# Optimization experiments

Hardware: AMD Instinct MI355X
Metric: run time of the kernel (lower is better)

## Reference

```python
import jax, jax.numpy as jnp
import numpy as np

B, N, D, C, H, W = 4, 900, 256, 256, 200, 200
HEADS, LVLS, PTS, K = 8, 1, 4, 10


def setup_inputs() -> dict:
    key = jax.random.key(0)
    ks = jax.random.split(key, 16)
    s = 0.02
    return {
        "query_embed": jax.random.normal(ks[0], (B, N, D), jnp.float32),
        "ctrl_points": jax.random.uniform(ks[1], (B, N, 4, 2), jnp.float32, -50.0, 50.0),
        "bev_features": jax.random.normal(ks[2], (B, C, H, W), jnp.float32),
        "spatial_shapes": jnp.array([[H, W]], dtype=jnp.int32),
        "pc_range": jnp.array([-51.2, -51.2, -5.0, 51.2, 51.2, 3.0], jnp.float32),
        "Wq": s * jax.random.normal(ks[3], (D, D)), "bq": jnp.zeros((D,)),
        "Wv": s * jax.random.normal(ks[4], (C, D)), "bv": jnp.zeros((D,)),
        "Woff": s * jax.random.normal(ks[5], (D, HEADS * LVLS * PTS * 2)), "boff": jnp.zeros((HEADS * LVLS * PTS * 2,)),
        "Wattn": s * jax.random.normal(ks[6], (D, HEADS * LVLS * PTS)), "battn": jnp.zeros((HEADS * LVLS * PTS,)),
        "Wmo": s * jax.random.normal(ks[7], (D, D)), "bmo": jnp.zeros((D,)),
        "Wo": s * jax.random.normal(ks[8], (D, D)), "bo": jnp.zeros((D,)),
    }


def _forward(query_embed, ctrl_points, bev_features, spatial_shapes, pc_range,
             Wq, bq, Wv, bv, Woff, boff, Wattn, battn, Wmo, bmo, Wo, bo):
    b, n, d = query_embed.shape
    _, c, h, w = bev_features.shape
    hd = d // HEADS

    # --- cubic Bezier interpolation: (B,N,4,2) -> (B,N,K,2) dense points ---
    t = jnp.linspace(0.0, 1.0, K, dtype=query_embed.dtype)
    basis = jnp.stack([(1 - t) ** 3, 3 * (1 - t) ** 2 * t, 3 * (1 - t) * t ** 2, t ** 3], axis=-1)  # (K,4)
    dense = jnp.einsum('kc,bncd->bnkd', basis, ctrl_points)
    # --- normalize to [0,1] by pc_range, clamp to [0.01,0.99] ---
    nx = (dense[..., 0] - pc_range[0]) / (pc_range[3] - pc_range[0])
    ny = (dense[..., 1] - pc_range[1]) / (pc_range[4] - pc_range[1])
    ref = jnp.clip(jnp.stack([nx, ny], axis=-1), 0.01, 0.99)  # (B,N,K,2)

    # --- projections ---
    q = query_embed @ Wq + bq                                       # (B,N,D) (identity for residual)
    v = bev_features.reshape(b, c, h * w).transpose(0, 2, 1) @ Wv + bv  # (B,HW,D)
    v = v.reshape(b, h * w, HEADS, hd)

    off = (q @ Woff + boff).reshape(b, n, HEADS, LVLS, PTS, 2)
    aw = jax.nn.softmax((q @ Wattn + battn).reshape(b, n, HEADS, LVLS * PTS), axis=-1)
    aw = aw.reshape(b, n, HEADS, PTS)  # LVLS == 1

    # offset normalizer = (W, H) per level
    normalizer = jnp.stack([spatial_shapes[..., 1], spatial_shapes[..., 0]], axis=-1).astype(q.dtype)  # (L,2)
    # sampling locations: broadcast K bezier points against heads/points offsets
    loc = ref[:, :, None, :, None, :] + off / normalizer[None, None, None, :, None, :]  # (B,N,HEADS,K,PTS,2)

    # --- bilinear sampling, align_corners=False, zero padding ---
    gx = loc[..., 0] * w - 0.5
    gy = loc[..., 1] * h - 0.5
    x0 = jnp.floor(gx)
    y0 = jnp.floor(gy)
    wx = gx - x0
    wy = gy - y0
    x0i = x0.astype(jnp.int32)
    y0i = y0.astype(jnp.int32)

    vflat = v.transpose(0, 2, 1, 3).reshape(b * HEADS, h * w, hd)  # (B*HEADS, HW, hd)

    def flat(a):  # (B,N,HEADS,K,PTS) -> (B*HEADS, N*K*PTS)
        return a.transpose(0, 2, 1, 3, 4).reshape(b * HEADS, n * K * PTS)

    acc = jnp.zeros((b * HEADS, n * K * PTS, hd), dtype=q.dtype)
    for dx, dy in ((0, 0), (1, 0), (0, 1), (1, 1)):
        ix = flat(x0i) + dx
        iy = flat(y0i) + dy
        wxx = flat(wx) if dx else (1.0 - flat(wx))
        wyy = flat(wy) if dy else (1.0 - flat(wy))
        valid = (ix >= 0) & (ix < w) & (iy >= 0) & (iy < h)
        idx = jnp.clip(iy, 0, h - 1) * w + jnp.clip(ix, 0, w - 1)
        corner = jnp.take_along_axis(vflat, idx[..., None], axis=1)  # (B*HEADS, Npts, hd)
        acc = acc + corner * (wxx * wyy * valid.astype(q.dtype))[..., None]

    sampled = acc.reshape(b, HEADS, n, K, PTS, hd)
    # weighted sum over (K, PTS); attention weights shared across the K bezier points
    out = jnp.einsum('bhnkpd,bnhp->bnhd', sampled, aw).reshape(b, n, d)
    out = out @ Wmo + bmo + q   # mmcv MSDeformAttn output_proj + residual (identity = query)
    out = out @ Wo + bo         # outer output_proj
    return out


def reference(query_embed, ctrl_points, bev_features, spatial_shapes, pc_range,
              Wq, bq, Wv, bv, Woff, boff, Wattn, battn, Wmo, bmo, Wo, bo):
    return _forward(query_embed, ctrl_points, bev_features, spatial_shapes, pc_range,
                    Wq, bq, Wv, bv, Woff, boff, Wattn, battn, Wmo, bmo, Wo, bo)
```

## Files before the change

kernel.cpp:

```cpp
#include <hip/hip_runtime.h>
#include <hip/hip_bf16.h>
#include <math.h>


typedef unsigned short u16;
typedef unsigned int u32;
typedef short bf16x8 __attribute__((ext_vector_type(8)));
typedef float f32x4 __attribute__((ext_vector_type(4)));

__device__ __forceinline__ float bflo(u32 w) {
  union { u32 i; float f; } c; c.i = w << 16; return c.f;
}
__device__ __forceinline__ float bfhi(u32 w) {
  union { u32 i; float f; } c; c.i = w & 0xffff0000u; return c.f;
}
__device__ __forceinline__ u16 f2bf(float f) {
  union { float f; u32 i; } c; c.f = f;
  u32 u = c.i;
  return (u16)((u + 0x7FFFu + ((u >> 16) & 1u)) >> 16);
}
__device__ __forceinline__ int imin(int a, int b) { return a < b ? a : b; }
__device__ __forceinline__ int imax(int a, int b) { return a > b ? a : b; }

__device__ __forceinline__ void glds16(const u16* g, u16* l) {
  __builtin_amdgcn_global_load_lds(
      (__attribute__((address_space(1))) const void*)g,
      (__attribute__((address_space(3))) void*)l, 16, 0, 0);
}

__global__ __launch_bounds__(256) void prep_weights(
    const float* __restrict__ Wq, const float* __restrict__ Wv,
    const float* __restrict__ Woff, const float* __restrict__ Wattn,
    const float* __restrict__ Wmo, const float* __restrict__ Wo,
    const float* __restrict__ bq, const float* __restrict__ boff,
    const float* __restrict__ battn, const float* __restrict__ bmo,
    const float* __restrict__ bo, const float* __restrict__ query,
    u16* __restrict__ bqoaT, u16* __restrict__ wvT, u16* __restrict__ woCat,
    float* __restrict__ bcat, float* __restrict__ bprime,
    u16* __restrict__ qin)
{
  const int idx = blockIdx.x * 256 + threadIdx.x;
  {
    int i = idx * 4;
    float4 v = *(const float4*)(query + i);
    uint2 st;
    st.x = (u32)f2bf(v.x) | ((u32)f2bf(v.y) << 16);
    st.y = (u32)f2bf(v.z) | ((u32)f2bf(v.w) << 16);
    *(uint2*)(qin + i) = st;
  }
  if (idx < 65536) {
    int r = idx >> 8, c = idx & 255;
    bqoaT[idx] = f2bf(Wq[c * 256 + r]);
    wvT[idx]   = f2bf(Wv[c * 256 + r]);
  }
  if (idx < 24576) {
    int n = idx >> 8, k = idx & 255;
    const float* wq = Wq + k * 256;
    float s = 0.f;
    if (n < 64) {
      const float* wo = Woff + n;
#pragma unroll 4
      for (int c = 0; c < 256; c += 4) {
        float4 a = *(const float4*)(wq + c);
        s += a.x * wo[(c + 0) * 64] + a.y * wo[(c + 1) * 64] +
             a.z * wo[(c + 2) * 64] + a.w * wo[(c + 3) * 64];
      }
    } else {
      const float* wa = Wattn + (n - 64);
#pragma unroll 4
      for (int c = 0; c < 256; c += 4) {
        float4 a = *(const float4*)(wq + c);
        s += a.x * wa[(c + 0) * 32] + a.y * wa[(c + 1) * 32] +
             a.z * wa[(c + 2) * 32] + a.w * wa[(c + 3) * 32];
      }
    }
    bqoaT[65536 + idx] = f2bf(s);
  }
  if (idx < 131072) {
    int n = idx >> 9, k = idx & 511;
    float s;
    if (k >= 256) {
      s = Wo[(size_t)(k - 256) * 256 + n];
    } else {
      const float* wm = Wmo + k * 256;
      const float* wo = Wo + n;
      s = 0.f;
#pragma unroll 4
      for (int c = 0; c < 256; c += 4) {
        float4 a = *(const float4*)(wm + c);
        s += a.x * wo[(c + 0) * 256] + a.y * wo[(c + 1) * 256] +
             a.z * wo[(c + 2) * 256] + a.w * wo[(c + 3) * 256];
      }
    }
    woCat[idx] = f2bf(s);
  }
  if (idx >= 131072 && idx < 131328) {
    int n = idx - 131072;
    const float* wo = Wo + n;
    float s = bo[n];
    for (int c = 0; c < 256; ++c) s += bmo[c] * wo[c * 256];
    bprime[n] = s;
  }
  if (idx >= 131328 && idx < 131680) {
    int n = idx - 131328;
    if (n < 256) {
      bcat[n] = bq[n];
    } else {
      int j = n - 256;
      float s;
      if (j < 64) {
        const float* wo = Woff + j;
        s = boff[j];
        for (int c = 0; c < 256; ++c) s += bq[c] * wo[c * 64];
      } else {
        const float* wa = Wattn + (j - 64);
        s = battn[j - 64];
        for (int c = 0; c < 256; ++c) s += bq[c] * wa[c * 32];
      }
      bcat[n] = s;
    }
  }
}

enum { GM_F32 = 0, GM_SPLIT = 1 };

template <int MODE>
__global__ __launch_bounds__(256) void gemm_bt(
    const u16* __restrict__ A, const u16* __restrict__ Bt,
    const float* __restrict__ bias,
    u16* __restrict__ outb, float* __restrict__ outf,
    int M, int N, int K, int lda, int ldo)
{
  __shared__ __align__(16) u16 lA[128 * 32];
  __shared__ __align__(16) u16 lB[128 * 32];
  const int tid = threadIdx.x;
  const int wv = tid >> 6, lane = tid & 63;
  const int m0 = blockIdx.y * 128;
  const int n0 = blockIdx.x * 128;

  const int crow = lane >> 2;
  const int ckoff = (lane & 3) * 8;
  const int a1 = imin(m0 + wv * 16 + crow, M - 1);
  const int a2 = imin(m0 + (wv + 4) * 16 + crow, M - 1);
  const int b1 = imin(n0 + wv * 16 + crow, N - 1);
  const int b2 = imin(n0 + (wv + 4) * 16 + crow, N - 1);
  const u16* gA1 = A + (size_t)a1 * lda + ckoff;
  const u16* gA2 = A + (size_t)a2 * lda + ckoff;
  const u16* gB1 = Bt + (size_t)b1 * K + ckoff;
  const u16* gB2 = Bt + (size_t)b2 * K + ckoff;
  u16* lA1 = lA + wv * 512;  u16* lA2 = lA + (wv + 4) * 512;
  u16* lB1 = lB + wv * 512;  u16* lB2 = lB + (wv + 4) * 512;

  const int fm = (wv & 1) * 64, fn = (wv >> 1) * 64;
  const int fr = lane & 15, fk = (lane >> 4) * 8;

  f32x4 acc[4][4];
#pragma unroll
  for (int i = 0; i < 4; ++i)
#pragma unroll
    for (int j = 0; j < 4; ++j) acc[i][j] = (f32x4){0.f, 0.f, 0.f, 0.f};

  for (int k0 = 0; k0 < K; k0 += 32) {
    glds16(gA1 + k0, lA1);
    glds16(gA2 + k0, lA2);
    glds16(gB1 + k0, lB1);
    glds16(gB2 + k0, lB2);
    __syncthreads();
    bf16x8 af[4], bfv[4];
#pragma unroll
    for (int i = 0; i < 4; ++i)
      af[i] = *(const bf16x8*)&lA[(fm + i * 16 + fr) * 32 + fk];
#pragma unroll
    for (int j = 0; j < 4; ++j)
      bfv[j] = *(const bf16x8*)&lB[(fn + j * 16 + fr) * 32 + fk];
    __syncthreads();
#pragma unroll
    for (int i = 0; i < 4; ++i)
#pragma unroll
      for (int j = 0; j < 4; ++j)
        acc[i][j] = __builtin_amdgcn_mfma_f32_16x16x32_bf16(af[i], bfv[j], acc[i][j], 0, 0, 0);
  }

  const int quad = lane >> 4;
#pragma unroll
  for (int j = 0; j < 4; ++j) {
    const int n = n0 + fn + j * 16 + fr;
    const bool nok = (n < N);
    const float bcol = bias[nok ? n : 0];
#pragma unroll
    for (int i = 0; i < 4; ++i) {
      const int mb = m0 + fm + i * 16 + quad * 4;
#pragma unroll
      for (int r = 0; r < 4; ++r) {
        const int m = mb + r;
        if (m < M && nok) {
          float x = acc[i][j][r] + bcol;
          if (MODE == GM_F32) {
            outf[(size_t)m * ldo + n] = x;
          } else {
            if (n < 256) outb[(size_t)m * 512 + n] = f2bf(x);
            else outf[(size_t)m * 96 + (n - 256)] = x;
          }
        }
      }
    }
  }
}

#define LOADB(S, R0, R1, R2, R3)                                   \
  { const float* s2_ = src + (size_t)((S) * 32) * 40000;           \
    R0 = *(const float4*)(s2_);                                    \
    R1 = *(const float4*)(s2_ + 4);                                \
    R2 = *(const float4*)(s2_ + 40000);                            \
    R3 = *(const float4*)(s2_ + 40004); }

#define CVW8F(BUF, R0, R1, R2, R3)                                           \
  { u32* lbw_ = (u32*)(BUF); u32 pk_;                                        \
    asm("v_cvt_pk_bf16_f32 %0, %1, %2" : "=v"(pk_) : "v"(R0.x), "v"(R2.x)); \
    lbw_[(((wrow + 0) * 16 + wslot) ^ wxor)] = pk_;                          \
    asm("v_cvt_pk_bf16_f32 %0, %1, %2" : "=v"(pk_) : "v"(R0.y), "v"(R2.y)); \
    lbw_[(((wrow + 1) * 16 + wslot) ^ wxor)] = pk_;                          \
    asm("v_cvt_pk_bf16_f32 %0, %1, %2" : "=v"(pk_) : "v"(R0.z), "v"(R2.z)); \
    lbw_[(((wrow + 2) * 16 + wslot) ^ wxor)] = pk_;                          \
    asm("v_cvt_pk_bf16_f32 %0, %1, %2" : "=v"(pk_) : "v"(R0.w), "v"(R2.w)); \
    lbw_[(((wrow + 3) * 16 + wslot) ^ wxor)] = pk_;                          \
    asm("v_cvt_pk_bf16_f32 %0, %1, %2" : "=v"(pk_) : "v"(R1.x), "v"(R3.x)); \
    lbw_[(((wrow + 4) * 16 + wslot) ^ wxor)] = pk_;                          \
    asm("v_cvt_pk_bf16_f32 %0, %1, %2" : "=v"(pk_) : "v"(R1.y), "v"(R3.y)); \
    lbw_[(((wrow + 5) * 16 + wslot) ^ wxor)] = pk_;                          \
    asm("v_cvt_pk_bf16_f32 %0, %1, %2" : "=v"(pk_) : "v"(R1.z), "v"(R3.z)); \
    lbw_[(((wrow + 6) * 16 + wslot) ^ wxor)] = pk_;                          \
    asm("v_cvt_pk_bf16_f32 %0, %1, %2" : "=v"(pk_) : "v"(R1.w), "v"(R3.w)); \
    lbw_[(((wrow + 7) * 16 + wslot) ^ wxor)] = pk_; }

__global__ __launch_bounds__(256) void gemm_v4(
    const u16* __restrict__ A,
    const float* __restrict__ bev,
    const float* __restrict__ bias,
    u16* __restrict__ outb,
    int zbase)
{
  const int tid = threadIdx.x;
  const int wv = tid >> 6, lane = tid & 63;
  const int z = zbase + blockIdx.y;
  const int w = blockIdx.x * 4 + wv;
  if (w >= 1250) return;
  const int nw0 = w * 32;
  const int fr = lane & 15, fk = (lane >> 4) * 8;

  const float* bsrc = bev + ((size_t)z * 256 + fk) * 40000 + nw0 + fr;
  const u16* asrc = A + (size_t)fr * 256 + fk;

  f32x4 acc[16][2];
#pragma unroll
  for (int i = 0; i < 16; ++i) {
    acc[i][0] = (f32x4){0.f, 0.f, 0.f, 0.f};
    acc[i][1] = (f32x4){0.f, 0.f, 0.f, 0.f};
  }

#pragma unroll
  for (int t = 0; t < 8; ++t) {
    const float* bs = bsrc + (size_t)(t * 32) * 40000;
    float b0[8], b1[8];
#pragma unroll
    for (int j = 0; j < 8; ++j) {
      b0[j] = bs[(size_t)j * 40000];
      b1[j] = bs[(size_t)j * 40000 + 16];
    }
    union { u32 u[4]; bf16x8 v; } p0, p1;
#pragma unroll
    for (int j = 0; j < 4; ++j) {
      asm("v_cvt_pk_bf16_f32 %0, %1, %2"
          : "=v"(p0.u[j]) : "v"(b0[2 * j]), "v"(b0[2 * j + 1]));
      asm("v_cvt_pk_bf16_f32 %0, %1, %2"
          : "=v"(p1.u[j]) : "v"(b1[2 * j]), "v"(b1[2 * j + 1]));
    }
#pragma unroll
    for (int i = 0; i < 16; ++i) {
      bf16x8 af = *(const bf16x8*)(asrc + i * 4096 + t * 32);
      acc[i][0] = __builtin_amdgcn_mfma_f32_16x16x32_bf16(af, p0.v, acc[i][0], 0, 0, 0);
      acc[i][1] = __builtin_amdgcn_mfma_f32_16x16x32_bf16(af, p1.v, acc[i][1], 0, 0, 0);
    }
  }

  const int quad = lane >> 4;
#pragma unroll
  for (int i = 0; i < 16; ++i) {
    const int mb = i * 16 + quad * 4;
#pragma unroll
    for (int j = 0; j < 2; ++j) {
      const int n = nw0 + j * 16 + fr;
      u16 u0 = f2bf(acc[i][j][0] + bias[mb + 0]);
      u16 u1 = f2bf(acc[i][j][1] + bias[mb + 1]);
      u16 u2 = f2bf(acc[i][j][2] + bias[mb + 2]);
      u16 u3 = f2bf(acc[i][j][3] + bias[mb + 3]);
      size_t off = (size_t)z * (8ull * 40000 * 32) +
                   (size_t)(mb >> 5) * (40000 * 32) + (size_t)n * 32 + (mb & 31);
      uint2 st; st.x = (u32)u0 | ((u32)u1 << 16); st.y = (u32)u2 | ((u32)u3 << 16);
      *(uint2*)(outb + off) = st;
    }
  }
}

__global__ __launch_bounds__(256, 2) void gemm_v(
    const u16* __restrict__ A, const float* __restrict__ bev,
    const float* __restrict__ bias, u16* __restrict__ outb, int zbase)
{
  __shared__ __align__(16) u16 lA[8 * 128 * 32];
  __shared__ __align__(16) u16 lB[2][128 * 32];
  const int tid = threadIdx.x;
  const int wv = tid >> 6, lane = tid & 63;
  const int m0 = blockIdx.x * 128;
  const int n0 = blockIdx.y * 128;
  const int z = zbase + blockIdx.z;

  const int crow = lane >> 2, ckoff = (lane & 3) * 8;
  const u16* gA1 = A + (size_t)(m0 + wv * 16 + crow) * 256 + ckoff;
  const u16* gA2 = A + (size_t)(m0 + (wv + 4) * 16 + crow) * 256 + ckoff;
  u16* lA1 = lA + wv * 512;
  u16* lA2 = lA + (wv + 4) * 512;

  const int kp = tid >> 4, nb = tid & 15;
  const int cb = imin(n0 + nb * 8, 40000 - 8);
  const float* src = bev + ((size_t)z * 256 + 2 * kp) * 40000 + cb;
  const int wslot = (((kp >> 2) ^ (nb & 3)) << 2) + (kp & 3);
  const int wxor = ((nb >> 2) & 1) << 4;
  const int wrow = nb * 8;

  const int fm = (wv & 1) * 64, fn = (wv >> 1) * 64;
  const int fr = lane & 15, fk = (lane >> 4) * 8;

  f32x4 acc[4][4];
#pragma unroll
  for (int i = 0; i < 4; ++i)
#pragma unroll
    for (int j = 0; j < 4; ++j) acc[i][j] = (f32x4){0.f, 0.f, 0.f, 0.f};

  float4 s0a, s0b, s0c, s0d, s1a, s1b, s1c, s1d;
  float4 s2a, s2b, s2c, s2d, s3a, s3b, s3c, s3d;

  LOADB(0, s0a, s0b, s0c, s0d);
#pragma unroll
  for (int s = 0; s < 8; ++s) {
    glds16(gA1 + s * 32, lA1 + s * 4096);
    glds16(gA2 + s * 32, lA2 + s * 4096);
  }
  LOADB(1, s1a, s1b, s1c, s1d);
  LOADB(2, s2a, s2b, s2c, s2d);
  LOADB(3, s3a, s3b, s3c, s3d);
  asm volatile("" ::: "memory");
  CVW8F(lB[0], s0a, s0b, s0c, s0d);
  __syncthreads();

#pragma unroll
  for (int t = 0; t < 8; ++t) {
    bf16x8 af[4], bfv[4];
#pragma unroll
    for (int i = 0; i < 4; ++i)
      af[i] = *(const bf16x8*)&lA[t * 4096 + (fm + i * 16 + fr) * 32 + fk];
#pragma unroll
    for (int j = 0; j < 4; ++j) {
      const int n = fn + j * 16 + fr;
      const int pc = (((lane >> 4) ^ ((n >> 3) & 3)) << 3);
      const int ri = (n * 32 + pc) ^ (((n >> 5) & 1) << 5);
      bfv[j] = *(const bf16x8*)&lB[t & 1][ri];
    }
    if (t == 0)      { LOADB(4, s0a, s0b, s0c, s0d); }
    else if (t == 1) { LOADB(5, s1a, s1b, s1c, s1d); }
    else if (t == 2) { LOADB(6, s2a, s2b, s2c, s2d); }
    else if (t == 3) { LOADB(7, s3a, s3b, s3c, s3d); }
    if (t == 0)      { CVW8F(lB[1], s1a, s1b, s1c, s1d); }
    else if (t == 1) { CVW8F(lB[0], s2a, s2b, s2c, s2d); }
    else if (t == 2) { CVW8F(lB[1], s3a, s3b, s3c, s3d); }
    else if (t == 3) { CVW8F(lB[0], s0a, s0b, s0c, s0d); }
    else if (t == 4) { CVW8F(lB[1], s1a, s1b, s1c, s1d); }
    else if (t == 5) { CVW8F(lB[0], s2a, s2b, s2c, s2d); }
    else if (t == 6) { CVW8F(lB[1], s3a, s3b, s3c, s3d); }
#pragma unroll
    for (int i = 0; i < 4; ++i)
#pragma unroll
      for (int j = 0; j < 4; ++j)
        acc[i][j] = __builtin_amdgcn_mfma_f32_16x16x32_bf16(af[i], bfv[j], acc[i][j], 0, 0, 0);
    if (t < 7) {
      __builtin_amdgcn_sched_barrier(0);
      asm volatile("s_waitcnt lgkmcnt(0)" ::: "memory");
      __builtin_amdgcn_sched_barrier(0);
      __builtin_amdgcn_s_barrier();
      __builtin_amdgcn_sched_barrier(0);
    }
  }

  const int quad = lane >> 4;
#pragma unroll
  for (int j = 0; j < 4; ++j) {
    const int n = n0 + fn + j * 16 + fr;
    if (n < 40000) {
#pragma unroll
      for (int i = 0; i < 4; ++i) {
        const int mb = m0 + fm + i * 16 + quad * 4;
        u16 u0 = f2bf(acc[i][j][0] + bias[mb + 0]);
        u16 u1 = f2bf(acc[i][j][1] + bias[mb + 1]);
        u16 u2 = f2bf(acc[i][j][2] + bias[mb + 2]);
        u16 u3 = f2bf(acc[i][j][3] + bias[mb + 3]);
        size_t off = (size_t)z * (8ull * 40000 * 32) +
                     (size_t)(mb >> 5) * (40000 * 32) + (size_t)n * 32 + (mb & 31);
        uint2 st; st.x = (u32)u0 | ((u32)u1 << 16); st.y = (u32)u2 | ((u32)u3 << 16);
        *(uint2*)(outb + off) = st;
      }
    }
  }
}

__global__ __launch_bounds__(256) void sampler(
    const float* __restrict__ ctrl,
    const float* __restrict__ pc,
    const float* __restrict__ oa_,
    const u16* __restrict__ v,
    u16* __restrict__ attn_out)
{
  __shared__ int   sX0[4][40], sY0[4][40];
  __shared__ float sWx[4][40], sWy[4][40], sAw[4][40];
  const int w = threadIdx.x >> 6, lane = threadIdx.x & 63;
  const int bh = blockIdx.x & 31;
  const int n = (blockIdx.x >> 5) * 4 + w;
  const int h = bh & 7, b = bh >> 3;
  const int row = b * 900 + n;

  if (lane < 40) {
    const int k = lane >> 2, p = lane & 3;
    const float t = (float)k * (1.0f / 9.0f), u = 1.f - t;
    const float c0 = u * u * u, c1 = 3.f * u * u * t, c2 = 3.f * u * t * t, c3 = t * t * t;
    const float* cp = ctrl + (size_t)row * 8;
    float cx = c0 * cp[0] + c1 * cp[2] + c2 * cp[4] + c3 * cp[6];
    float cy = c0 * cp[1] + c1 * cp[3] + c2 * cp[5] + c3 * cp[7];
    float nx = (cx - pc[0]) / (pc[3] - pc[0]);
    float ny = (cy - pc[1]) / (pc[4] - pc[1]);
    nx = fminf(fmaxf(nx, 0.01f), 0.99f);
    ny = fminf(fmaxf(ny, 0.01f), 0.99f);
    const float* oa = oa_ + (size_t)row * 96;
    float ox = oa[h * 8 + p * 2 + 0], oy = oa[h * 8 + p * 2 + 1];
    float l0 = oa[64 + h * 4 + 0], l1 = oa[64 + h * 4 + 1];
    float l2 = oa[64 + h * 4 + 2], l3 = oa[64 + h * 4 + 3];
    float mx = fmaxf(fmaxf(l0, l1), fmaxf(l2, l3));
    float e0 = __expf(l0 - mx), e1 = __expf(l1 - mx), e2 = __expf(l2 - mx), e3 = __expf(l3 - mx);
    float lp = (p == 0) ? l0 : (p == 1) ? l1 : (p == 2) ? l2 : l3;
    float aw = __expf(lp - mx) / (e0 + e1 + e2 + e3);
    float gx = (nx + ox * (1.f / 200.f)) * 200.f - 0.5f;
    float gy = (ny + oy * (1.f / 200.f)) * 200.f - 0.5f;
    float x0 = floorf(gx), y0 = floorf(gy);
    sX0[w][lane] = (int)x0; sY0[w][lane] = (int)y0;
    sWx[w][lane] = gx - x0; sWy[w][lane] = gy - y0; sAw[w][lane] = aw;
  }
  __syncthreads();

  const int sg = lane >> 3;
  const int ch0 = (lane & 7) * 4;
  const u16* vb = v + ((size_t)(b * 8 + h)) * (40000 * 32) + ch0;
  float a0 = 0.f, a1 = 0.f, a2 = 0.f, a3 = 0.f;
#pragma unroll
  for (int p = 0; p < 5; ++p) {
    const int s = p * 8 + sg;
    const int x0 = sX0[w][s], y0 = sY0[w][s];
    const float wx = sWx[w][s], wy = sWy[w][s], aw = sAw[w][s];
    const int x1 = x0 + 1, y1 = y0 + 1;
    const int cx0 = imin(imax(x0, 0), 199), cx1 = imin(imax(x1, 0), 199);
    const int cy0 = imin(imax(y0, 0), 199), cy1 = imin(imax(y1, 0), 199);
    const bool vx0 = (u32)x0 < 200u, vx1 = (u32)x1 < 200u;
    const bool vy0 = (u32)y0 < 200u, vy1 = (u32)y1 < 200u;
    const float w00 = (vx0 && vy0) ? aw * (1.f - wx) * (1.f - wy) : 0.f;
    const float w10 = (vx1 && vy0) ? aw * wx * (1.f - wy) : 0.f;
    const float w01 = (vx0 && vy1) ? aw * (1.f - wx) * wy : 0.f;
    const float w11 = (vx1 && vy1) ? aw * wx * wy : 0.f;
    uint2 d00 = *(const uint2*)(vb + (size_t)(cy0 * 200 + cx0) * 32);
    uint2 d10 = *(const uint2*)(vb + (size_t)(cy0 * 200 + cx1) * 32);
    uint2 d01 = *(const uint2*)(vb + (size_t)(cy1 * 200 + cx0) * 32);
    uint2 d11 = *(const uint2*)(vb + (size_t)(cy1 * 200 + cx1) * 32);
    a0 += w00 * bflo(d00.x) + w10 * bflo(d10.x) + w01 * bflo(d01.x) + w11 * bflo(d11.x);
    a1 += w00 * bfhi(d00.x) + w10 * bfhi(d10.x) + w01 * bfhi(d01.x) + w11 * bfhi(d11.x);
    a2 += w00 * bflo(d00.y) + w10 * bflo(d10.y) + w01 * bflo(d01.y) + w11 * bflo(d11.y);
    a3 += w00 * bfhi(d00.y) + w10 * bfhi(d10.y) + w01 * bfhi(d01.y) + w11 * bfhi(d11.y);
  }
#pragma unroll
  for (int off = 8; off < 64; off <<= 1) {
    a0 += __shfl_xor(a0, off);
    a1 += __shfl_xor(a1, off);
    a2 += __shfl_xor(a2, off);
    a3 += __shfl_xor(a3, off);
  }
  if (lane < 8) {
    uint2 st;
    st.x = (u32)f2bf(a0) | ((u32)f2bf(a1) << 16);
    st.y = (u32)f2bf(a2) | ((u32)f2bf(a3) << 16);
    *(uint2*)(attn_out + (size_t)row * 512 + h * 32 + ch0) = st;
  }
}

extern "C" void kernel_launch(void* const* d_in, const int* in_sizes, int n_in,
                              void* d_out, int out_size, void* d_ws, size_t ws_size,
                              hipStream_t stream)
{
  const float* query = (const float*)d_in[0];
  const float* ctrl  = (const float*)d_in[1];
  const float* bev   = (const float*)d_in[2];
  const float* pc    = (const float*)d_in[4];
  const float* Wq    = (const float*)d_in[5];  const float* bq    = (const float*)d_in[6];
  const float* Wv    = (const float*)d_in[7];  const float* bv    = (const float*)d_in[8];
  const float* Woff  = (const float*)d_in[9];  const float* boff  = (const float*)d_in[10];
  const float* Wattn = (const float*)d_in[11]; const float* battn = (const float*)d_in[12];
  const float* Wmo   = (const float*)d_in[13]; const float* bmo   = (const float*)d_in[14];
  const float* Wo    = (const float*)d_in[15]; const float* bo    = (const float*)d_in[16];

  char* ws = (char*)d_ws;
  size_t off = 0;
  auto alloc = [&](size_t bytes) -> void* {
    void* p = ws + off; off += (bytes + 255) & ~(size_t)255; return p;
  };
  u16*  v     = (u16*)alloc(4ull * 8 * 40000 * 32 * 2);
  u16*  qin   = (u16*)alloc(3600ull * 256 * 2);
  u16*  wvT   = (u16*)alloc(65536 * 2);
  u16*  bqoaT = (u16*)alloc(352 * 256 * 2);
  u16*  woCat = (u16*)alloc(256 * 512 * 2);
  float* bcat = (float*)alloc(352 * 4);
  float* bprime = (float*)alloc(256 * 4);
  float* oaf  = (float*)alloc(3600ull * 96 * 4);
  u16*  qcat  = (u16*)alloc(3600ull * 512 * 2);
  (void)ws_size; (void)in_sizes; (void)n_in; (void)out_size;

  prep_weights<<<900, 256, 0, stream>>>(Wq, Wv, Woff, Wattn, Wmo, Wo,
                                        bq, boff, battn, bmo, bo, query,
                                        bqoaT, wvT, woCat, bcat, bprime, qin);
  gemm_v4<<<dim3(313, 2), 256, 0, stream>>>(wvT, bev, bv, v, 0);
  gemm_v<<<dim3(2, 313, 2), 256, 0, stream>>>(wvT, bev, bv, v, 2);
  gemm_bt<GM_SPLIT><<<dim3(3, 29), 256, 0, stream>>>(
      qin, bqoaT, bcat, qcat + 256, oaf, 3600, 352, 256, 256, 0);
  sampler<<<7200, 256, 0, stream>>>(ctrl, pc, oaf, v, qcat);
  gemm_bt<GM_F32><<<dim3(2, 29), 256, 0, stream>>>(
      qcat, woCat, bprime, nullptr, (float*)d_out, 3600, 256, 512, 512, 256);
}
```

Baseline: 437.6 us.

## Stage Wv tile in LDS and split value GEMM over M halves

The value-projection kernel for the first two batches now splits the 256 output channels into two 128-row blocks and copies the matching weight slice into shared memory once per block. Before, each wave read all 256 weight rows straight from global memory. This halves the per-wave accumulator count, which should raise occupancy, and moves weight reads to LDS. In exchange, every BEV column tile is now read and converted twice, once per M half, and the last tile clamps its column start so it overlaps the previous one.

```diff
diff --git a/kernel.cpp b/kernel.cpp
--- a/kernel.cpp
+++ b/kernel.cpp
@@ -233,27 +233,37 @@
     asm("v_cvt_pk_bf16_f32 %0, %1, %2" : "=v"(pk_) : "v"(R1.w), "v"(R3.w)); \
     lbw_[(((wrow + 7) * 16 + wslot) ^ wxor)] = pk_; }
 
-__global__ __launch_bounds__(256) void gemm_v4(
+__global__ __launch_bounds__(256) void gemm_v5(
     const u16* __restrict__ A,
     const float* __restrict__ bev,
     const float* __restrict__ bias,
     u16* __restrict__ outb,
     int zbase)
 {
+  __shared__ __align__(16) u16 lA[8 * 128 * 32];
   const int tid = threadIdx.x;
   const int wv = tid >> 6, lane = tid & 63;
-  const int z = zbase + blockIdx.y;
-  const int w = blockIdx.x * 4 + wv;
-  if (w >= 1250) return;
-  const int nw0 = w * 32;
+  const int m0 = blockIdx.x * 128;
+  const int n0 = blockIdx.y * 128;
+  const int z = zbase + blockIdx.z;
+  const int nw0 = imin(n0 + wv * 32, 40000 - 32);
+
+  const int crow = lane >> 2, ckoff = (lane & 3) * 8;
+  const u16* gA1 = A + (size_t)(m0 + wv * 16 + crow) * 256 + ckoff;
+  const u16* gA2 = A + (size_t)(m0 + (wv + 4) * 16 + crow) * 256 + ckoff;
+#pragma unroll
+  for (int s = 0; s < 8; ++s) {
+    glds16(gA1 + s * 32, lA + wv * 512 + s * 4096);
+    glds16(gA2 + s * 32, lA + (wv + 4) * 512 + s * 4096);
+  }
+  __syncthreads();
+
   const int fr = lane & 15, fk = (lane >> 4) * 8;
-
   const float* bsrc = bev + ((size_t)z * 256 + fk) * 40000 + nw0 + fr;
-  const u16* asrc = A + (size_t)fr * 256 + fk;
-
-  f32x4 acc[16][2];
-#pragma unroll
-  for (int i = 0; i < 16; ++i) {
+
+  f32x4 acc[8][2];
+#pragma unroll
+  for (int i = 0; i < 8; ++i) {
     acc[i][0] = (f32x4){0.f, 0.f, 0.f, 0.f};
     acc[i][1] = (f32x4){0.f, 0.f, 0.f, 0.f};
   }
@@ -263,21 +273,21 @@
     const float* bs = bsrc + (size_t)(t * 32) * 40000;
     float b0[8], b1[8];
 #pragma unroll
-    for (int j = 0; j < 8; ++j) {
-      b0[j] = bs[(size_t)j * 40000];
-      b1[j] = bs[(size_t)j * 40000 + 16];
+    for (int jj = 0; jj < 8; ++jj) {
+      b0[jj] = bs[(size_t)jj * 40000];
+      b1[jj] = bs[(size_t)jj * 40000 + 16];
     }
     union { u32 u[4]; bf16x8 v; } p0, p1;
 #pragma unroll
-    for (int j = 0; j < 4; ++j) {
+    for (int q = 0; q < 4; ++q) {
       asm("v_cvt_pk_bf16_f32 %0, %1, %2"
-          : "=v"(p0.u[j]) : "v"(b0[2 * j]), "v"(b0[2 * j + 1]));
+          : "=v"(p0.u[q]) : "v"(b0[2 * q]), "v"(b0[2 * q + 1]));
       asm("v_cvt_pk_bf16_f32 %0, %1, %2"
-          : "=v"(p1.u[j]) : "v"(b1[2 * j]), "v"(b1[2 * j + 1]));
-    }
-#pragma unroll
-    for (int i = 0; i < 16; ++i) {
-      bf16x8 af = *(const bf16x8*)(asrc + i * 4096 + t * 32);
+          : "=v"(p1.u[q]) : "v"(b1[2 * q]), "v"(b1[2 * q + 1]));
+    }
+#pragma unroll
+    for (int i = 0; i < 8; ++i) {
+      bf16x8 af = *(const bf16x8*)&lA[t * 4096 + (i * 16 + fr) * 32 + fk];
       acc[i][0] = __builtin_amdgcn_mfma_f32_16x16x32_bf16(af, p0.v, acc[i][0], 0, 0, 0);
       acc[i][1] = __builtin_amdgcn_mfma_f32_16x16x32_bf16(af, p1.v, acc[i][1], 0, 0, 0);
     }
@@ -285,15 +295,15 @@
 
   const int quad = lane >> 4;
 #pragma unroll
-  for (int i = 0; i < 16; ++i) {
-    const int mb = i * 16 + quad * 4;
+  for (int i = 0; i < 8; ++i) {
+    const int mb = m0 + i * 16 + quad * 4;
 #pragma unroll
     for (int j = 0; j < 2; ++j) {
       const int n = nw0 + j * 16 + fr;
-      u16 u0 = f2bf(acc[i][j][0] + bias[mb + 0]);
-      u16 u1 = f2bf(acc[i][j][1] + bias[mb + 1]);
-      u16 u2 = f2bf(acc[i][j][2] + bias[mb + 2]);
-      u16 u3 = f2bf(acc[i][j][3] + bias[mb + 3]);
+      u16 u0 = f2bf(acc[i][j][0] + bias[(mb & 255) + 0]);
+      u16 u1 = f2bf(acc[i][j][1] + bias[(mb & 255) + 1]);
+      u16 u2 = f2bf(acc[i][j][2] + bias[(mb & 255) + 2]);
+      u16 u3 = f2bf(acc[i][j][3] + bias[(mb & 255) + 3]);
       size_t off = (size_t)z * (8ull * 40000 * 32) +
                    (size_t)(mb >> 5) * (40000 * 32) + (size_t)n * 32 + (mb & 31);
       uint2 st; st.x = (u32)u0 | ((u32)u1 << 16); st.y = (u32)u2 | ((u32)u3 << 16);
@@ -529,7 +539,7 @@
   prep_weights<<<900, 256, 0, stream>>>(Wq, Wv, Woff, Wattn, Wmo, Wo,
                                         bq, boff, battn, bmo, bo, query,
                                         bqoaT, wvT, woCat, bcat, bprime, qin);
-  gemm_v4<<<dim3(313, 2), 256, 0, stream>>>(wvT, bev, bv, v, 0);
+  gemm_v5<<<dim3(2, 313, 2), 256, 0, stream>>>(wvT, bev, bv, v, 0);
   gemm_v<<<dim3(2, 313, 2), 256, 0, stream>>>(wvT, bev, bv, v, 2);
   gemm_bt<GM_SPLIT><<<dim3(3, 29), 256, 0, stream>>>(
       qin, bqoaT, bcat, qcat + 256, oaf, 3600, 352, 256, 256, 0);
```

Measured after the change: 392.0 us. -10.4%, faster.
